# Kernel optimization log

Measured on AMD Instinct MI355X. Metric: run time of the kernel, lower is better.

Reference implementation:

```python
import jax, jax.numpy as jnp
import numpy as np

EPS = 1e-12


def setup_inputs() -> dict:
    key = jax.random.key(0)
    k1, k2 = jax.random.split(key)
    N, K, D = 32768, 2048, 512
    node_repr = jax.random.normal(k1, (N, D), dtype=jnp.float32)
    mask = jnp.ones((N, 1), dtype=jnp.float32)
    # nn.Embedding weight for the centroids (euclidean branch: exp_map_zero is identity)
    centroid_weight = jax.random.normal(k2, (K, D), dtype=jnp.float32)
    return {"node_repr": node_repr, "mask": mask, "centroid_weight": centroid_weight}


def reference(node_repr, mask, centroid_weight):
    # Euclidean manifold: exp_map_zero(x) = x; distance(x, y) = ||x - y||_2.
    # The torch code expands to [N*K, D]; here we fuse via the Gram-matrix identity
    x2 = jnp.sum(node_repr * node_repr, axis=-1, keepdims=True)        # [N, 1]
    c2 = jnp.sum(centroid_weight * centroid_weight, axis=-1)           # [K]
    xc = jnp.einsum('nd,kd->nk', node_repr, centroid_weight)           # [N, K] GEMM
    d2 = x2 + c2[None, :] - 2.0 * xc                                   # [N, K]
    dist = jnp.sqrt(jnp.maximum(d2, EPS))                              # [N, K]
    node_centroid_dist = dist[None, :, :] * mask[None, :, :]           # [1, N, K] (mask broadcasts [1,N,1])
    graph_centroid_dist = jnp.sum(node_centroid_dist, axis=1) / jnp.sum(mask)  # [1, K]
    return graph_centroid_dist, node_centroid_dist
```

## Files before the change

kernel.cpp:

```cpp
#include <hip/hip_runtime.h>
#include <hip/hip_bf16.h>
#include <math.h>

typedef __bf16 bf16_t;
typedef __bf16 bf16x4 __attribute__((ext_vector_type(4)));
typedef __bf16 bf16x8 __attribute__((ext_vector_type(8)));
typedef float floatx4 __attribute__((ext_vector_type(4)));

#define N_NODES 32768
#define K_CENT  2048
#define D_DIM   512

__global__ void prep_rows_kernel(const float* __restrict__ src,
                                 bf16_t* __restrict__ dst,
                                 float* __restrict__ sq) {
  const int w = threadIdx.x >> 6;
  const int l = threadIdx.x & 63;
  const int row = blockIdx.x * 4 + w;
  const float4* s = (const float4*)(src + (size_t)row * D_DIM);
  float4 f0 = s[l];
  float4 f1 = s[64 + l];
  bf16x4 b0 = { (bf16_t)f0.x, (bf16_t)f0.y, (bf16_t)f0.z, (bf16_t)f0.w };
  bf16x4 b1 = { (bf16_t)f1.x, (bf16_t)f1.y, (bf16_t)f1.z, (bf16_t)f1.w };
  bf16x4* d = (bf16x4*)(dst + (size_t)row * D_DIM);
  d[l] = b0;
  d[64 + l] = b1;
  float v = f0.x*f0.x + f0.y*f0.y + f0.z*f0.z + f0.w*f0.w
          + f1.x*f1.x + f1.y*f1.y + f1.z*f1.z + f1.w*f1.w;
  #pragma unroll
  for (int s2 = 32; s2; s2 >>= 1) v += __shfl_xor(v, s2);
  if (l == 0) sq[row] = v;
}

__global__ void mask_sum_kernel(const float* __restrict__ m,
                                float* __restrict__ out, int n) {
  float v = 0.f;
  for (int i = blockIdx.x * blockDim.x + threadIdx.x; i < n;
       i += gridDim.x * blockDim.x)
    v += m[i];
  #pragma unroll
  for (int s = 32; s; s >>= 1) v += __shfl_xor(v, s);
  __shared__ float red[4];
  if ((threadIdx.x & 63) == 0) red[threadIdx.x >> 6] = v;
  __syncthreads();
  if (threadIdx.x == 0) atomicAdd(out, red[0] + red[1] + red[2] + red[3]);
}

__device__ inline void gld_lds16(const void* g, void* l) {
  __builtin_amdgcn_global_load_lds(
      (__attribute__((address_space(1))) void*)const_cast<void*>(g),
      (__attribute__((address_space(3))) void*)l, 16, 0, 0);
}

__global__ void __launch_bounds__(256)
gemm_dist_kernel(const bf16_t* __restrict__ A,
                 const bf16_t* __restrict__ B,
                 const float* __restrict__ x2,
                 const float* __restrict__ c2,
                 const float* __restrict__ mask,
                 float* __restrict__ out_node,
                 float* __restrict__ colsum) {
  __shared__ __align__(16) bf16_t sA[128 * 64];
  __shared__ __align__(16) bf16_t sB[128 * 64];

  const int t = threadIdx.x;
  const int w = t >> 6;
  const int l = t & 63;
  const int bm = blockIdx.y;
  const int bn = blockIdx.x;
  const int wm = (w >> 1) * 64;
  const int wn = (w & 1) * 64;
  const int lr = l & 15;
  const int lk = (l >> 4) * 8;

  floatx4 acc[4][4] = {};

  const int srow = w * 8 + (l >> 3);
  const int scol = (l & 7) * 8;
  const bf16_t* gA = A + (size_t)(bm * 128 + srow) * D_DIM + scol;
  const bf16_t* gB = B + (size_t)(bn * 128 + srow) * D_DIM + scol;
  char* lA = (char*)sA + w * 1024;
  char* lB = (char*)sB + w * 1024;

  for (int kt = 0; kt < D_DIM; kt += 64) {
    #pragma unroll
    for (int p = 0; p < 4; ++p) {
      gld_lds16(gA + (size_t)(p * 32) * D_DIM + kt, lA + p * 4096);
      gld_lds16(gB + (size_t)(p * 32) * D_DIM + kt, lB + p * 4096);
    }
    __syncthreads();
    #pragma unroll
    for (int ks = 0; ks < 64; ks += 32) {
      bf16x8 af[4], bfr[4];
      #pragma unroll
      for (int i = 0; i < 4; ++i)
        af[i] = *(const bf16x8*)&sA[(wm + i * 16 + lr) * 64 + ks + lk];
      #pragma unroll
      for (int j = 0; j < 4; ++j)
        bfr[j] = *(const bf16x8*)&sB[(wn + j * 16 + lr) * 64 + ks + lk];
      #pragma unroll
      for (int i = 0; i < 4; ++i) {
        #pragma unroll
        for (int j = 0; j < 4; ++j)
          acc[i][j] = __builtin_amdgcn_mfma_f32_16x16x32_bf16(
              af[i], bfr[j], acc[i][j], 0, 0, 0);
      }
    }
    __syncthreads();
  }

  const int col0 = bn * 128 + wn;
  float c2v[4];
  #pragma unroll
  for (int j = 0; j < 4; ++j) c2v[j] = c2[col0 + j * 16 + lr];

  float colacc[4] = {0.f, 0.f, 0.f, 0.f};
  #pragma unroll
  for (int i = 0; i < 4; ++i) {
    const int rbase = bm * 128 + wm + i * 16 + (l >> 4) * 4;
    #pragma unroll
    for (int r = 0; r < 4; ++r) {
      const int row = rbase + r;
      const float xv = x2[row];
      const float mk = mask[row];
      float* orow = out_node + (size_t)row * K_CENT + col0 + lr;
      #pragma unroll
      for (int j = 0; j < 4; ++j) {
        float d2 = xv + c2v[j] - 2.0f * acc[i][j][r];
        float dist = sqrtf(fmaxf(d2, 1e-12f));
        float dm = dist * mk;
        orow[j * 16] = dm;
        colacc[j] += dm;
      }
    }
  }

  #pragma unroll
  for (int j = 0; j < 4; ++j) {
    colacc[j] += __shfl_xor(colacc[j], 16);
    colacc[j] += __shfl_xor(colacc[j], 32);
  }
  float* colbuf = (float*)sA;
  if (w < 2 && l < 16) {
    #pragma unroll
    for (int j = 0; j < 4; ++j) colbuf[wn + j * 16 + l] = colacc[j];
  }
  __syncthreads();
  if (w >= 2 && l < 16) {
    #pragma unroll
    for (int j = 0; j < 4; ++j) colbuf[wn + j * 16 + l] += colacc[j];
  }
  __syncthreads();
  if (t < 128) atomicAdd(&colsum[bn * 128 + t], colbuf[t]);
}

__global__ void finalize_kernel(const float* __restrict__ colsum,
                                const float* __restrict__ msum,
                                float* __restrict__ out) {
  int k = blockIdx.x * 256 + threadIdx.x;
  out[k] = colsum[k] / msum[0];
}

extern "C" void kernel_launch(void* const* d_in, const int* in_sizes, int n_in,
                              void* d_out, int out_size, void* d_ws, size_t ws_size,
                              hipStream_t stream) {
  const float* node = (const float*)d_in[0];
  const float* mask = (const float*)d_in[1];
  const float* cent = (const float*)d_in[2];
  float* out_graph = (float*)d_out;
  float* out_node  = out_graph + K_CENT;

  char* ws = (char*)d_ws;
  size_t off = 0;
  bf16_t* Abf = (bf16_t*)(ws + off); off += (size_t)N_NODES * D_DIM * sizeof(bf16_t);
  bf16_t* Cbf = (bf16_t*)(ws + off); off += (size_t)K_CENT * D_DIM * sizeof(bf16_t);
  float* x2     = (float*)(ws + off); off += (size_t)N_NODES * sizeof(float);
  float* c2     = (float*)(ws + off); off += (size_t)K_CENT * sizeof(float);
  float* colsum = (float*)(ws + off); off += (size_t)K_CENT * sizeof(float);
  float* msum   = (float*)(ws + off); off += sizeof(float);

  hipMemsetAsync(colsum, 0, (K_CENT + 1) * sizeof(float), stream);

  prep_rows_kernel<<<N_NODES / 4, 256, 0, stream>>>(node, Abf, x2);
  prep_rows_kernel<<<K_CENT / 4, 256, 0, stream>>>(cent, Cbf, c2);
  mask_sum_kernel<<<64, 256, 0, stream>>>(mask, msum, N_NODES);
  gemm_dist_kernel<<<dim3(16, 256), 256, 0, stream>>>(
      Abf, Cbf, x2, c2, mask, out_node, colsum);
  finalize_kernel<<<K_CENT / 256, 256, 0, stream>>>(colsum, msum, out_graph);
}
```

Baseline: 422.0 us.

## Double-buffer LDS tiles, XOR-swizzle LDS layout, remap blocks per XCD, nontemporal stores

Splits the GEMM K-loop into two LDS buffers so the next tile's global-to-LDS load overlaps the MFMA work on the current tile, with one barrier per iteration. It XOR-swizzles column chunks in LDS to avoid bank conflicts on the fragment reads. It also remaps the 1D block index so consecutive blocks on the same XCD share A rows, and writes the 256MB distance output with nontemporal stores. The cost is doubled LDS use, which may lower occupancy.

```diff
diff --git a/kernel.cpp b/kernel.cpp
--- a/kernel.cpp
+++ b/kernel.cpp
@@ -52,6 +52,18 @@
       (__attribute__((address_space(3))) void*)l, 16, 0, 0);
 }
 
+__device__ __forceinline__ void stage_tile(const bf16_t* gA, const bf16_t* gB,
+                                           bf16_t* sAb, bf16_t* sBb,
+                                           int w, int kt) {
+  char* lA = (char*)sAb + w * 1024;
+  char* lB = (char*)sBb + w * 1024;
+  #pragma unroll
+  for (int p = 0; p < 4; ++p) {
+    gld_lds16(gA + (size_t)(p * 32) * D_DIM + kt, lA + p * 4096);
+    gld_lds16(gB + (size_t)(p * 32) * D_DIM + kt, lB + p * 4096);
+  }
+}
+
 __global__ void __launch_bounds__(256)
 gemm_dist_kernel(const bf16_t* __restrict__ A,
                  const bf16_t* __restrict__ B,
@@ -60,44 +72,54 @@
                  const float* __restrict__ mask,
                  float* __restrict__ out_node,
                  float* __restrict__ colsum) {
-  __shared__ __align__(16) bf16_t sA[128 * 64];
-  __shared__ __align__(16) bf16_t sB[128 * 64];
+  __shared__ __align__(16) bf16_t sA[2][128 * 64];
+  __shared__ __align__(16) bf16_t sB[2][128 * 64];
 
   const int t = threadIdx.x;
   const int w = t >> 6;
   const int l = t & 63;
-  const int bm = blockIdx.y;
-  const int bn = blockIdx.x;
+
+  const int wg = (blockIdx.x & 7) * 512 + (blockIdx.x >> 3);
+  const int bm = wg >> 4;
+  const int bn = wg & 15;
+
   const int wm = (w >> 1) * 64;
   const int wn = (w & 1) * 64;
   const int lr = l & 15;
-  const int lk = (l >> 4) * 8;
+  const int hi = l >> 4;
 
   floatx4 acc[4][4] = {};
 
   const int srow = w * 8 + (l >> 3);
-  const int scol = (l & 7) * 8;
+  const int scol = ((l & 7) ^ (l >> 3)) * 8;
   const bf16_t* gA = A + (size_t)(bm * 128 + srow) * D_DIM + scol;
   const bf16_t* gB = B + (size_t)(bn * 128 + srow) * D_DIM + scol;
-  char* lA = (char*)sA + w * 1024;
-  char* lB = (char*)sB + w * 1024;
-
-  for (int kt = 0; kt < D_DIM; kt += 64) {
-    #pragma unroll
-    for (int p = 0; p < 4; ++p) {
-      gld_lds16(gA + (size_t)(p * 32) * D_DIM + kt, lA + p * 4096);
-      gld_lds16(gB + (size_t)(p * 32) * D_DIM + kt, lB + p * 4096);
-    }
-    __syncthreads();
-    #pragma unroll
-    for (int ks = 0; ks < 64; ks += 32) {
+
+  stage_tile(gA, gB, sA[0], sB[0], w, 0);
+  __syncthreads();
+
+  int cur = 0;
+  for (int tk = 0; tk < 8; ++tk) {
+    if (tk < 7)
+      stage_tile(gA, gB, sA[cur ^ 1], sB[cur ^ 1], w, (tk + 1) * 64);
+
+    const char* cAb = (const char*)sA[cur];
+    const char* cBb = (const char*)sB[cur];
+    #pragma unroll
+    for (int ks = 0; ks < 2; ++ks) {
       bf16x8 af[4], bfr[4];
       #pragma unroll
-      for (int i = 0; i < 4; ++i)
-        af[i] = *(const bf16x8*)&sA[(wm + i * 16 + lr) * 64 + ks + lk];
-      #pragma unroll
-      for (int j = 0; j < 4; ++j)
-        bfr[j] = *(const bf16x8*)&sB[(wn + j * 16 + lr) * 64 + ks + lk];
+      for (int i = 0; i < 4; ++i) {
+        const int r = wm + i * 16 + lr;
+        const int c = ((ks * 4 + hi) ^ (lr & 7)) * 16;
+        af[i] = *(const bf16x8*)(cAb + r * 128 + c);
+      }
+      #pragma unroll
+      for (int j = 0; j < 4; ++j) {
+        const int r = wn + j * 16 + lr;
+        const int c = ((ks * 4 + hi) ^ (lr & 7)) * 16;
+        bfr[j] = *(const bf16x8*)(cBb + r * 128 + c);
+      }
       #pragma unroll
       for (int i = 0; i < 4; ++i) {
         #pragma unroll
@@ -107,6 +129,7 @@
       }
     }
     __syncthreads();
+    cur ^= 1;
   }
 
   const int col0 = bn * 128 + wn;
@@ -117,7 +140,7 @@
   float colacc[4] = {0.f, 0.f, 0.f, 0.f};
   #pragma unroll
   for (int i = 0; i < 4; ++i) {
-    const int rbase = bm * 128 + wm + i * 16 + (l >> 4) * 4;
+    const int rbase = bm * 128 + wm + i * 16 + hi * 4;
     #pragma unroll
     for (int r = 0; r < 4; ++r) {
       const int row = rbase + r;
@@ -129,7 +152,7 @@
         float d2 = xv + c2v[j] - 2.0f * acc[i][j][r];
         float dist = sqrtf(fmaxf(d2, 1e-12f));
         float dm = dist * mk;
-        orow[j * 16] = dm;
+        __builtin_nontemporal_store(dm, &orow[j * 16]);
         colacc[j] += dm;
       }
     }
@@ -184,7 +207,7 @@
   prep_rows_kernel<<<N_NODES / 4, 256, 0, stream>>>(node, Abf, x2);
   prep_rows_kernel<<<K_CENT / 4, 256, 0, stream>>>(cent, Cbf, c2);
   mask_sum_kernel<<<64, 256, 0, stream>>>(mask, msum, N_NODES);
-  gemm_dist_kernel<<<dim3(16, 256), 256, 0, stream>>>(
+  gemm_dist_kernel<<<4096, 256, 0, stream>>>(
       Abf, Cbf, x2, c2, mask, out_node, colsum);
   finalize_kernel<<<K_CENT / 256, 256, 0, stream>>>(colsum, msum, out_graph);
 }
```

New measurement: 451.7 us. 7.0% more time.
